# Performance work log

Hardware: AMD Instinct MI355X
Metric: run time of the kernel (lower is better)

## Reference

```python
import jax, jax.numpy as jnp
import numpy as np
from math import pi as PI, lgamma, log

_B = 64  # bandlimit
_BATCH = 512


def _little_half(B):
    # Wigner little-d at beta = pi/2 via three-term recurrence (float64).
    c = B - 1
    d = np.zeros((B, 2 * B - 1, 2 * B - 1))
    s2 = np.sqrt(2.0)
    d[0, c, c] = 1.0
    d[1, c - 1, c - 1] = 0.5
    d[1, c - 1, c] = 1.0 / s2
    d[1, c - 1, c + 1] = 0.5
    d[1, c, c - 1] = -1.0 / s2
    d[1, c, c + 1] = 1.0 / s2
    d[1, c + 1, c - 1] = 0.5
    d[1, c + 1, c] = -1.0 / s2
    d[1, c + 1, c + 1] = 0.5
    for l in range(2, B):
        for m in range(0, l):
            for n in range(0, l):
                if m == 0 and n == 0:
                    d[l, c, c] = -1.0 * ((l - 1) / l) * d[l - 2, c, c]
                else:
                    denom = (-1 + l) * np.sqrt((l - m) * (l + m) * (l - n) * (l + n))
                    c1 = (1 - 2 * l) * m * n / denom
                    c2 = -1.0 * l * np.sqrt(((l - 1) ** 2 - m * m) * ((l - 1) ** 2 - n * n)) / denom
                    d[l, m + c, n + c] = c1 * d[l - 1, m + c, n + c] + c2 * d[l - 2, m + c, n + c]
        for m in range(0, l + 1):
            lnV = 0.5 * (lgamma(2 * l + 1) - lgamma(l + m + 1) - lgamma(l - m + 1)) - l * log(2.0)
            d[l, m + c, l + c] = np.exp(lnV)
            d[l, l + c, m + c] = ((-1.0) ** (l - m)) * np.exp(lnV)
        for m in range(0, l + 1):
            for n in range(0, l + 1):
                val = d[l, m + c, n + c]
                if m != 0 or n != 0:
                    d[l, -m + c, -n + c] = ((-1.0) ** (m - n)) * val
                    d[l, -m + c, n + c] = ((-1.0) ** (l - n)) * val
                    d[l, m + c, -n + c] = ((-1.0) ** (l + m)) * val
    return d


def _wigner_coeffs(B):
    # Sparse COO for D: [B*(2B-1), 2B*(2B-1)], block per order m.
    d = _little_half(B)
    c = B - 1
    N = 2 * B
    rows, cols, vals = [], [], []
    H = 0
    W = 0
    for m in range(-(B - 1), B):
        for l in range(abs(m), B):
            for n in range(0, l + 1):
                if m % 2 == 0:
                    cc = np.sqrt((2 * l + 1) / 2.0) * np.sqrt(N if n == 0 else 2.0 * N)
                    if m % 4 == 2:
                        cc *= -1.0
                    coeff = cc * d[l, n + c, -m + c] * d[l, n + c, c]
                elif n == l:
                    coeff = 0.0
                else:
                    cc = np.sqrt((2 * l + 1) / 2.0) * np.sqrt(2.0 * N)
                    if m % 4 == 1:
                        cc *= -1.0
                    coeff = cc * d[l, n + 1 + c, -m + c] * d[l, n + 1 + c, c]
                if abs(coeff) > 1e-15:
                    rows.append(l + H)
                    cols.append(n + W)
                    vals.append(coeff)
        H += B
        W += N
    return np.asarray(rows, np.int32), np.asarray(cols, np.int32), np.asarray(vals)


def _dlt_weights(B):
    k = np.arange(2 * B)[:, None]
    p = np.arange(B)[None, :]
    C = (2.0 / B) * np.sin(PI * (2 * k[:, 0] + 1) / (4.0 * B))
    wk = np.sum(np.sin((2 * k + 1) * (2 * p + 1) * PI / (4.0 * B)) / (2 * p + 1), axis=1)
    return C * wk


def _idct_matrix(N):
    k = np.arange(N)[:, None]
    n = np.arange(N)[None, :]
    DI = np.cos(PI * n * (k + 0.5) / N)
    DI[:, 0] *= np.sqrt(1.0 / N)
    DI[:, 1:] *= np.sqrt(2.0 / N)
    return DI


def _idst_matrix(N):
    k = np.arange(N)[:, None]
    n = np.arange(N)[None, :]
    DI = np.sin(PI * (n + 1) * (k + 0.5) / N)
    DI[:, N - 1] = (-1.0) ** np.arange(N)
    DI[:, N - 1] *= np.sqrt(1.0 / N)
    DI[:, : N - 1] *= np.sqrt(2.0 / N)
    return DI


def setup_inputs() -> dict:
    B = _B
    key = jax.random.key(0)
    psiHat = jax.random.normal(key, (_BATCH, 2 * B - 1, 2 * B), dtype=jnp.float32)
    m = np.arange(-(B - 1), B)
    Cm = ((-1.0) ** m) * np.sqrt(2.0 * PI)
    Wdiag = _dlt_weights(B)
    XFc = Wdiag[:, None] * _idct_matrix(2 * B)  # y = x @ XFc (nn.Linear with weight=XF.T)
    XFs = Wdiag[:, None] * _idst_matrix(2 * B)
    D_row, D_col, D_val = _wigner_coeffs(B)
    return {
        "psiHat": psiHat,
        "Cm": jnp.asarray(Cm, jnp.float32),
        "XFc": jnp.asarray(XFc, jnp.float32),
        "XFs": jnp.asarray(XFs, jnp.float32),
        "D_val": jnp.asarray(D_val, jnp.float32),
        "D_row": jnp.asarray(D_row),
        "D_col": jnp.asarray(D_col),
    }


def reference(psiHat, Cm, XFc, XFs, D_val, D_row, D_col):
    b, M, twoB = psiHat.shape  # M = 2B-1
    B = twoB // 2
    if (B - 1) % 2 == 1:
        cInd = np.arange(1, 2 * B - 1, 2)
        sInd = np.arange(0, 2 * B - 1, 2)
    else:
        sInd = np.arange(1, 2 * B - 1, 2)
        cInd = np.arange(0, 2 * B - 1, 2)
    psi = Cm[None, :, None] * psiHat
    psi = psi.at[:, cInd, :].set(psi[:, cInd, :] @ XFc)
    psi = psi.at[:, sInd, :].set(psi[:, sInd, :] @ XFs)
    x = psi.reshape(b, twoB * M).T  # [2B*(2B-1), b]
    # sparse mm: D @ x via gather + segment-sum over rows
    y = jax.ops.segment_sum(D_val[:, None] * x[D_col], D_row, num_segments=B * M)
    return y.reshape(M, B, b).transpose(2, 0, 1)  # [b, 2B-1, B]
```

## Files before the change

kernel.cpp:

```cpp
#include <hip/hip_runtime.h>
#include <hip/hip_bf16.h>


#define B_     64
#define M_     127
#define TWOB_  128

using bf16x8 = __attribute__((ext_vector_type(8))) short;
using f32x4  = __attribute__((ext_vector_type(4))) float;

__device__ inline short f2bf(float x) {
    __hip_bfloat16 h = __float2bfloat16(x);
    return *reinterpret_cast<short*>(&h);
}

__device__ inline int wave_lb(const int* __restrict__ arr, int n, int target, int lane) {
    int a = 0, w = n;
    while (w > 64) {
        int step = (w + 63) >> 6;
        int off  = lane * step;
        bool inr = (off < w);
        int p    = a + (inr ? off : 0);
        int v    = (inr && p < n) ? arr[p] : 0x7fffffff;
        unsigned long long mask = __ballot(v < target);
        int c = __popcll(mask);
        int a2 = (c > 0) ? (a + (c - 1) * step + 1) : a;
        int U  = (c * step < w) ? (a + c * step) : (a + w);
        a = a2;
        w = U - a2;
        if (w < 0) w = 0;
    }
    bool lt = (lane < w) && (a + lane < n) && (arr[a + lane] < target);
    return a + __popcll(__ballot(lt));
}

__global__ __launch_bounds__(256, 4) void fdlt_fused(
    const float* __restrict__ psiHat,
    const float* __restrict__ Cm,
    const float* __restrict__ XFc,
    const float* __restrict__ XFs,
    const float* __restrict__ Dval,
    const int*   __restrict__ Drow,
    const int*   __restrict__ Dcol,
    int nnz,
    float* __restrict__ out)
{
    __shared__ short EmL[B_ * TWOB_];
    __shared__ short As [B_ * TWOB_];
    __shared__ short Dmb[B_ * B_];

    const int bid  = blockIdx.x;
    const int xcd  = bid & 7;
    const int rest = bid >> 3;
    const int m    = xcd + ((rest & 15) << 3);
    const int tile = rest >> 4;
    if (m >= M_) return;
    const int b0 = tile * 64;
    const int t  = threadIdx.x;

    const int lane = t & 63;
    const int w    = t >> 6;
    const int lr   = lane & 15;
    const int lg   = lane >> 4;

    f32x4 pre[8];
    #pragma unroll
    for (int j = 0; j < 4; ++j) {
        int unit = t + j * 256;
        int row  = unit >> 4;
        int u    = unit & 15;
        const float* src = psiHat + ((size_t)(b0 + row) * M_ + m) * TWOB_ + u * 8;
        pre[2 * j]     = __builtin_nontemporal_load(reinterpret_cast<const f32x4*>(src));
        pre[2 * j + 1] = __builtin_nontemporal_load(reinterpret_cast<const f32x4*>(src + 4));
    }

    const float* __restrict__ XF = (m & 1) ? XFc : XFs;
    f32x4 xfp[2][2][2];
    #pragma unroll
    for (int ks = 0; ks < 2; ++ks)
        #pragma unroll
        for (int kt2 = 0; kt2 < 2; ++kt2) {
            const float* ap = XF + (size_t)((w * 2 + kt2) * 16 + lr) * TWOB_ + ks * 32 + lg * 8;
            xfp[ks][kt2][0] = *reinterpret_cast<const f32x4*>(ap);
            xfp[ks][kt2][1] = *reinterpret_cast<const f32x4*>(ap + 4);
        }

    {
        uint4 z = make_uint4(0, 0, 0, 0);
        uint4* p = reinterpret_cast<uint4*>(Dmb);
        p[t] = z;
        p[t + 256] = z;
    }

    const int lo = wave_lb(Drow, nnz, m * B_, lane);
    const int hi = wave_lb(Drow, nnz, (m + 1) * B_, lane);

    int   rr[9], cc[9];
    float vv[9];
    bool  ok[9];
    #pragma unroll
    for (int j = 0; j < 9; ++j) {
        int i  = lo + t + j * 256;
        ok[j]  = (i < hi);
        int ic = i < nnz ? i : (nnz - 1);
        rr[j] = Drow[ic];
        cc[j] = Dcol[ic];
        vv[j] = Dval[ic];
    }
    __syncthreads();

    #pragma unroll
    for (int j = 0; j < 9; ++j) {
        if (ok[j]) {
            int l = rr[j] - m * B_;
            int n = cc[j] - m * TWOB_;
            int u = n >> 3;
            Dmb[l * B_ + (((u ^ (l & 7)) << 3) | (n & 7))] = f2bf(vv[j]);
        }
    }
    __syncthreads();

    const float cm = Cm[m];

    f32x4 bacc[2][4];
    #pragma unroll
    for (int kt2 = 0; kt2 < 2; ++kt2)
        #pragma unroll
        for (int lt = 0; lt < 4; ++lt) bacc[kt2][lt] = (f32x4){0.f, 0.f, 0.f, 0.f};

    #pragma unroll
    for (int ks = 0; ks < 2; ++ks) {
        bf16x8 af[2];
        #pragma unroll
        for (int kt2 = 0; kt2 < 2; ++kt2) {
            af[kt2][0] = f2bf(xfp[ks][kt2][0][0]); af[kt2][1] = f2bf(xfp[ks][kt2][0][1]);
            af[kt2][2] = f2bf(xfp[ks][kt2][0][2]); af[kt2][3] = f2bf(xfp[ks][kt2][0][3]);
            af[kt2][4] = f2bf(xfp[ks][kt2][1][0]); af[kt2][5] = f2bf(xfp[ks][kt2][1][1]);
            af[kt2][6] = f2bf(xfp[ks][kt2][1][2]); af[kt2][7] = f2bf(xfp[ks][kt2][1][3]);
        }
        #pragma unroll
        for (int lt = 0; lt < 4; ++lt) {
            int l = lt * 16 + lr;
            int g = ks * 4 + lg;
            bf16x8 bfr = *reinterpret_cast<const bf16x8*>(Dmb + l * B_ + ((g ^ (l & 7)) << 3));
            bacc[0][lt] = __builtin_amdgcn_mfma_f32_16x16x32_bf16(af[0], bfr, bacc[0][lt], 0, 0, 0);
            bacc[1][lt] = __builtin_amdgcn_mfma_f32_16x16x32_bf16(af[1], bfr, bacc[1][lt], 0, 0, 0);
        }
    }
    #pragma unroll
    for (int kt2 = 0; kt2 < 2; ++kt2) {
        #pragma unroll
        for (int lt = 0; lt < 4; ++lt) {
            int l  = lt * 16 + lr;
            int k0 = (w * 2 + kt2) * 16 + lg * 4;
            unsigned short h0 = (unsigned short)f2bf(cm * bacc[kt2][lt][0]);
            unsigned short h1 = (unsigned short)f2bf(cm * bacc[kt2][lt][1]);
            unsigned short h2 = (unsigned short)f2bf(cm * bacc[kt2][lt][2]);
            unsigned short h3 = (unsigned short)f2bf(cm * bacc[kt2][lt][3]);
            uint2 pack;
            pack.x = (unsigned)h0 | ((unsigned)h1 << 16);
            pack.y = (unsigned)h2 | ((unsigned)h3 << 16);
            int u    = k0 >> 3;
            int half = (k0 >> 2) & 1;
            *reinterpret_cast<uint2*>(EmL + l * TWOB_ + ((u ^ (l & 15)) << 3) + (half << 2)) = pack;
        }
    }

    #pragma unroll
    for (int j = 0; j < 4; ++j) {
        int unit = t + j * 256;
        int row  = unit >> 4;
        int u    = unit & 15;
        bf16x8 s;
        s[0] = f2bf(pre[2*j][0]); s[1] = f2bf(pre[2*j][1]);
        s[2] = f2bf(pre[2*j][2]); s[3] = f2bf(pre[2*j][3]);
        s[4] = f2bf(pre[2*j+1][0]); s[5] = f2bf(pre[2*j+1][1]);
        s[6] = f2bf(pre[2*j+1][2]); s[7] = f2bf(pre[2*j+1][3]);
        *reinterpret_cast<bf16x8*>(As + row * TWOB_ + ((u ^ (row & 15)) << 3)) = s;
    }
    __syncthreads();

    f32x4 acc[4];
    #pragma unroll
    for (int nt = 0; nt < 4; ++nt) acc[nt] = (f32x4){0.f, 0.f, 0.f, 0.f};

    #pragma unroll
    for (int ks = 0; ks < 4; ++ks) {
        int l  = w * 16 + lr;
        int g2 = ks * 4 + lg;
        bf16x8 af = *reinterpret_cast<const bf16x8*>(EmL + l * TWOB_ + ((g2 ^ lr) << 3));
        #pragma unroll
        for (int nt = 0; nt < 4; ++nt) {
            int row = nt * 16 + lr;
            bf16x8 bfr = *reinterpret_cast<const bf16x8*>(As + row * TWOB_ + ((g2 ^ lr) << 3));
            acc[nt] = __builtin_amdgcn_mfma_f32_16x16x32_bf16(af, bfr, acc[nt], 0, 0, 0);
        }
    }

    #pragma unroll
    for (int nt = 0; nt < 4; ++nt) {
        int b = b0 + nt * 16 + lr;
        f32x4 v = acc[nt];
        __builtin_nontemporal_store(
            v, reinterpret_cast<f32x4*>(out + ((size_t)b * M_ + m) * B_ + w * 16 + lg * 4));
    }
}

extern "C" void kernel_launch(void* const* d_in, const int* in_sizes, int n_in,
                              void* d_out, int out_size, void* d_ws, size_t ws_size,
                              hipStream_t stream) {
    const float* psiHat = (const float*)d_in[0];
    const float* Cm     = (const float*)d_in[1];
    const float* XFc    = (const float*)d_in[2];
    const float* XFs    = (const float*)d_in[3];
    const float* Dval   = (const float*)d_in[4];
    const int*   Drow   = (const int*)d_in[5];
    const int*   Dcol   = (const int*)d_in[6];
    const int nnz = in_sizes[4];

    fdlt_fused<<<dim3(1024), dim3(256), 0, stream>>>(
        psiHat, Cm, XFc, XFs, Dval, Drow, Dcol, nnz, (float*)d_out);
}
```

Before: 20.69 us.

## Process two 64-batch tiles per block, reusing the per-order Wigner-DCT product

Each block now handles 128 batch rows instead of 64, and the grid is halved to 512 blocks. The per-m setup (binary search of the sparse rows, building the D block, the XF·D MFMA product into EmL) is computed once and its A-fragments are kept in registers for two output tiles. The second tile's psiHat load is issued before the first tile's GEMM so the global load overlaps compute. The cost is fewer blocks, hence less parallelism on a large GPU, plus an extra barrier and somewhat higher register use.

```diff
diff --git a/kernel.cpp b/kernel.cpp
--- a/kernel.cpp
+++ b/kernel.cpp
@@ -53,15 +53,16 @@
     const int xcd  = bid & 7;
     const int rest = bid >> 3;
     const int m    = xcd + ((rest & 15) << 3);
-    const int tile = rest >> 4;
+    const int tp   = rest >> 4;
     if (m >= M_) return;
-    const int b0 = tile * 64;
+    const int b0 = tp * 128;
     const int t  = threadIdx.x;
 
     const int lane = t & 63;
     const int w    = t >> 6;
     const int lr   = lane & 15;
     const int lg   = lane >> 4;
+
 
     f32x4 pre[8];
     #pragma unroll
@@ -178,31 +179,86 @@
         s[6] = f2bf(pre[2*j+1][2]); s[7] = f2bf(pre[2*j+1][3]);
         *reinterpret_cast<bf16x8*>(As + row * TWOB_ + ((u ^ (row & 15)) << 3)) = s;
     }
-    __syncthreads();
-
-    f32x4 acc[4];
-    #pragma unroll
-    for (int nt = 0; nt < 4; ++nt) acc[nt] = (f32x4){0.f, 0.f, 0.f, 0.f};
-
-    #pragma unroll
-    for (int ks = 0; ks < 4; ++ks) {
-        int l  = w * 16 + lr;
-        int g2 = ks * 4 + lg;
-        bf16x8 af = *reinterpret_cast<const bf16x8*>(EmL + l * TWOB_ + ((g2 ^ lr) << 3));
+
+    #pragma unroll
+    for (int j = 0; j < 4; ++j) {
+        int unit = t + j * 256;
+        int row  = unit >> 4;
+        int u    = unit & 15;
+        const float* src = psiHat + ((size_t)(b0 + 64 + row) * M_ + m) * TWOB_ + u * 8;
+        pre[2 * j]     = __builtin_nontemporal_load(reinterpret_cast<const f32x4*>(src));
+        pre[2 * j + 1] = __builtin_nontemporal_load(reinterpret_cast<const f32x4*>(src + 4));
+    }
+    __syncthreads();
+
+    bf16x8 eaf[4];
+    {
+        int l = w * 16 + lr;
+        #pragma unroll
+        for (int ks = 0; ks < 4; ++ks)
+            eaf[ks] = *reinterpret_cast<const bf16x8*>(
+                EmL + l * TWOB_ + (((ks * 4 + lg) ^ lr) << 3));
+    }
+
+    {
+        f32x4 acc[4];
+        #pragma unroll
+        for (int nt = 0; nt < 4; ++nt) acc[nt] = (f32x4){0.f, 0.f, 0.f, 0.f};
+        #pragma unroll
+        for (int ks = 0; ks < 4; ++ks) {
+            int g2 = ks * 4 + lg;
+            #pragma unroll
+            for (int nt = 0; nt < 4; ++nt) {
+                int row = nt * 16 + lr;
+                bf16x8 bfr = *reinterpret_cast<const bf16x8*>(As + row * TWOB_ + ((g2 ^ lr) << 3));
+                acc[nt] = __builtin_amdgcn_mfma_f32_16x16x32_bf16(eaf[ks], bfr, acc[nt], 0, 0, 0);
+            }
+        }
         #pragma unroll
         for (int nt = 0; nt < 4; ++nt) {
-            int row = nt * 16 + lr;
-            bf16x8 bfr = *reinterpret_cast<const bf16x8*>(As + row * TWOB_ + ((g2 ^ lr) << 3));
-            acc[nt] = __builtin_amdgcn_mfma_f32_16x16x32_bf16(af, bfr, acc[nt], 0, 0, 0);
-        }
-    }
-
-    #pragma unroll
-    for (int nt = 0; nt < 4; ++nt) {
-        int b = b0 + nt * 16 + lr;
-        f32x4 v = acc[nt];
-        __builtin_nontemporal_store(
-            v, reinterpret_cast<f32x4*>(out + ((size_t)b * M_ + m) * B_ + w * 16 + lg * 4));
+            int b = b0 + nt * 16 + lr;
+            f32x4 v = acc[nt];
+            __builtin_nontemporal_store(
+                v, reinterpret_cast<f32x4*>(out + ((size_t)b * M_ + m) * B_ + w * 16 + lg * 4));
+        }
+    }
+    __syncthreads();
+
+    #pragma unroll
+    for (int j = 0; j < 4; ++j) {
+        int unit = t + j * 256;
+        int row  = unit >> 4;
+        int u    = unit & 15;
+        bf16x8 s;
+        s[0] = f2bf(pre[2*j][0]); s[1] = f2bf(pre[2*j][1]);
+        s[2] = f2bf(pre[2*j][2]); s[3] = f2bf(pre[2*j][3]);
+        s[4] = f2bf(pre[2*j+1][0]); s[5] = f2bf(pre[2*j+1][1]);
+        s[6] = f2bf(pre[2*j+1][2]); s[7] = f2bf(pre[2*j+1][3]);
+        *reinterpret_cast<bf16x8*>(As + row * TWOB_ + ((u ^ (row & 15)) << 3)) = s;
+    }
+    __syncthreads();
+
+    {
+        f32x4 acc[4];
+        #pragma unroll
+        for (int nt = 0; nt < 4; ++nt) acc[nt] = (f32x4){0.f, 0.f, 0.f, 0.f};
+        #pragma unroll
+        for (int ks = 0; ks < 4; ++ks) {
+            int g2 = ks * 4 + lg;
+            #pragma unroll
+            for (int nt = 0; nt < 4; ++nt) {
+                int row = nt * 16 + lr;
+                bf16x8 bfr = *reinterpret_cast<const bf16x8*>(As + row * TWOB_ + ((g2 ^ lr) << 3));
+                acc[nt] = __builtin_amdgcn_mfma_f32_16x16x32_bf16(eaf[ks], bfr, acc[nt], 0, 0, 0);
+            }
+        }
+        #pragma unroll
+        for (int nt = 0; nt < 4; ++nt) {
+            int b = b0 + 64 + nt * 16 + lr;
+            f32x4 v = acc[nt];
+            __builtin_nontemporal_store(
+                v, reinterpret_cast<f32x4*>(out + ((size_t)b * M_ + m) * B_ + w * 16 + lg * 4));
+        }
     }
 }
 
@@ -218,6 +274,6 @@
     const int*   Dcol   = (const int*)d_in[6];
     const int nnz = in_sizes[4];
 
-    fdlt_fused<<<dim3(1024), dim3(256), 0, stream>>>(
+    fdlt_fused<<<dim3(512), dim3(256), 0, stream>>>(
         psiHat, Cm, XFc, XFs, Dval, Drow, Dcol, nnz, (float*)d_out);
 }
```

After: 20.74 us. No clear change (+0.2%).
